# Performance work log

Measured on AMD Instinct MI355X. Metric: run time of the kernel, lower is better.

## Reference

```python
import jax, jax.numpy as jnp
import numpy as np

# KroneckerLinear: W ~= sum_i (A_i kron B_i); efficient path computes, per token,
# Y = sum_i A_i @ X @ B_i^T with X = x.reshape(in1, in2), output flattened as (out1*out2).

IN1, IN2 = 64, 64      # in_factors (in1*in2 = in_features = 4096)
OUT1, OUT2 = 64, 64    # out_factors (out1*out2 = out_features = 4096)
NUM_SUM = 2
BATCH, SEQ = 4, 4096


def setup_inputs() -> dict:
    key = jax.random.key(0)
    kx, ka, kb, kbias = jax.random.split(key, 4)
    x = jax.random.normal(kx, (BATCH, SEQ, IN1 * IN2), dtype=jnp.float32)
    # kaiming-uniform-like scale for small factors
    bound_a = 1.0 / np.sqrt(IN1)
    bound_b = 1.0 / np.sqrt(IN2)
    A = jax.random.uniform(ka, (NUM_SUM, OUT1, IN1), dtype=jnp.float32, minval=-bound_a, maxval=bound_a)
    B = jax.random.uniform(kb, (NUM_SUM, OUT2, IN2), dtype=jnp.float32, minval=-bound_b, maxval=bound_b)
    bound = 1.0 / np.sqrt(IN1 * IN2)
    bias = jax.random.uniform(kbias, (OUT1 * OUT2,), dtype=jnp.float32, minval=-bound, maxval=bound)
    return {"x": x, "A": A, "B": B, "bias": bias}


def reference(x, A, B, bias):
    Bsz, T, _ = x.shape
    X = x.reshape(Bsz, T, IN1, IN2)  # (b, t, i, j)
    # y[b,t,o,p] = sum_s sum_ij A[s,o,i] * X[b,t,i,j] * B[s,p,j]  -> (out1, out2)
    y = jnp.einsum("btij,soi,spj->btop", X, A, B)
    return y.reshape(Bsz, T, OUT1 * OUT2) + bias
```

## Files before the change

kernel.cpp:

```cpp
#include <hip/hip_runtime.h>
#include <hip/hip_bf16.h>

typedef float  f32x4  __attribute__((ext_vector_type(4)));
typedef short  bf16x8 __attribute__((ext_vector_type(8)));

#define NT      16384
#define NBLOCK  256
#define TPS     (NT / NBLOCK)

__device__ __forceinline__ short f2bf(float x) {
  return (short)__builtin_bit_cast(unsigned short, __float2bfloat16(x));
}
__device__ __forceinline__ unsigned packbf2(float a, float b) {
  return (unsigned)(unsigned short)f2bf(a) | ((unsigned)(unsigned short)f2bf(b) << 16);
}

__device__ __forceinline__ void gload16(const float* gp, float* lp) {
  __builtin_amdgcn_global_load_lds((const __attribute__((address_space(1))) void*)gp,
                                   (__attribute__((address_space(3))) void*)lp,
                                   16, 0, 0);
}
__device__ __forceinline__ unsigned ldsaddr(const void* p) {
  return (unsigned)(uintptr_t)(const __attribute__((address_space(3))) void*)p;
}

__device__ __forceinline__ void stageQW(float* XB, const float* gbase, int j, int lane) {
#pragma unroll
  for (int qq = 0; qq < 4; ++qq) {
    const int q = j * 4 + qq;
    const int i = q * 4 + (lane >> 4);
    const float* gp = gbase + i * 64 + (((lane & 15) ^ (i & 7)) << 2);
    gload16(gp, XB + q * 256);
  }
}

__global__ __launch_bounds__(512, 1)
void kron_kernel(const float* __restrict__ x,
                 const float* __restrict__ A,
                 const float* __restrict__ Bm,
                 const float* __restrict__ bias,
                 float* __restrict__ out) {
  __shared__ float  xb[4][4096];
  __shared__ bf16x8 AT[1024];
  __shared__ bf16x8 BT[1024];
  __shared__ unsigned long long Ul[2][2048];

  const int tid  = threadIdx.x;
  const int lane = tid & 63;
  const int w    = tid >> 6;
  const int j    = w & 3;
  const int g    = lane >> 4;
  const int l15  = lane & 15;
  const int blk  = blockIdx.x;
  const bool consumer = (w < 4);

  f32x4 bv[4];
  if (consumer) {
#pragma unroll
    for (int t = 0; t < 4; ++t) {
      const int idx = j * 4 + t;
      const int s = idx >> 3, ot = (idx & 7) >> 1, c = idx & 1;
      const int o = ot * 16 + l15;
      bf16x8 v;
#pragma unroll
      for (int e = 0; e < 8; ++e) {
        const int i = c * 32 + 4 * g + (e & 3) + 16 * (e >> 2);
        v[e] = f2bf(A[s * 4096 + o * 64 + i]);
      }
      AT[idx * 64 + lane] = v;
    }
#pragma unroll
    for (int t = 0; t < 4; ++t) {
      const int idx = j * 4 + t;
      const int s = idx >> 3, pt = (idx & 7) >> 1, jc = idx & 1;
      const int p = pt * 16 + l15;
      bf16x8 v;
#pragma unroll
      for (int e = 0; e < 8; ++e)
        v[e] = f2bf(Bm[s * 4096 + p * 64 + (jc * 32 + 8 * g + e)]);
      BT[idx * 64 + lane] = v;
    }
#pragma unroll
    for (int ot = 0; ot < 4; ++ot)
      bv[ot] = *(const f32x4*)(bias + (ot * 16 + l15) * 64 + j * 16 + 4 * g);
  }
  __syncthreads();

  if (!consumer) {
    stageQW(&xb[0][0], x + ((size_t)blk << 12),            j, lane);
    stageQW(&xb[1][0], x + ((size_t)(blk + NBLOCK) << 12), j, lane);
    asm volatile("s_waitcnt vmcnt(4)" ::: "memory");
  }
  __builtin_amdgcn_s_barrier();

  const unsigned wsw = (unsigned)(2 * ((l15 >> 2) & 1));
  const unsigned q2  = (unsigned)((l15 >> 2) & 1);

  for (int k = 0; k <= TPS; ++k) {
    if (consumer) {
      f32x4 r0[2], r1[2];
      if (k < TPS) {
        const unsigned ba   = ldsaddr(&xb[k & 3][0]);
        const unsigned base = ba + (unsigned)(j * 16 + l15) * 256u;
        const unsigned m    = (unsigned)(l15 & 7);
#pragma unroll
        for (int jc = 0; jc < 2; ++jc) {
          const unsigned c0 = (unsigned)(8 * jc + 2 * g);
          asm volatile("ds_read_b128 %0, %1" : "=v"(r0[jc]) : "v"(base + ((c0 ^ m) << 4)) : "memory");
          asm volatile("ds_read_b128 %0, %1" : "=v"(r1[jc]) : "v"(base + (((c0 + 1u) ^ m) << 4)) : "memory");
        }
      }

      if (k > 0) {
        const unsigned long long* Up = &Ul[(k - 1) & 1][0];
        f32x4 acc[4];
#pragma unroll
        for (int ot = 0; ot < 4; ++ot) acc[ot] = bv[ot];
#pragma unroll
        for (int s = 0; s < 2; ++s) {
          bf16x8 uf[2];
#pragma unroll
          for (int c = 0; c < 2; ++c)
            uf[c] = *reinterpret_cast<const bf16x8*>(
                &Up[((((s * 4 + j) * 4 + g) * 16 + l15) << 2) + 2u * ((unsigned)c ^ q2)]);
#pragma unroll
          for (int ot = 0; ot < 4; ++ot)
#pragma unroll
            for (int c = 0; c < 2; ++c)
              acc[ot] = __builtin_amdgcn_mfma_f32_16x16x32_bf16(
                  uf[c], AT[(s * 8 + ot * 2 + c) * 64 + lane], acc[ot], 0, 0, 0);
        }
        float* ob = out + ((size_t)(blk + (k - 1) * NBLOCK) << 12);
#pragma unroll
        for (int ot = 0; ot < 4; ++ot)
          *(f32x4*)(ob + (ot * 16 + l15) * 64 + j * 16 + 4 * g) = acc[ot];
      }

      if (k < TPS) {
        asm volatile("s_waitcnt lgkmcnt(0)" ::: "memory");
        __builtin_amdgcn_sched_barrier(0);
        bf16x8 xf[2];
#pragma unroll
        for (int jc = 0; jc < 2; ++jc) {
          bf16x8 t;
          t[0]=f2bf(r0[jc][0]); t[1]=f2bf(r0[jc][1]); t[2]=f2bf(r0[jc][2]); t[3]=f2bf(r0[jc][3]);
          t[4]=f2bf(r1[jc][0]); t[5]=f2bf(r1[jc][1]); t[6]=f2bf(r1[jc][2]); t[7]=f2bf(r1[jc][3]);
          xf[jc] = t;
        }
        unsigned long long* Uw = &Ul[k & 1][0];
#pragma unroll
        for (int s = 0; s < 2; ++s) {
#pragma unroll
          for (int pt = 0; pt < 4; ++pt) {
            f32x4 a1 = (f32x4){0.f, 0.f, 0.f, 0.f};
#pragma unroll
            for (int jc = 0; jc < 2; ++jc)
              a1 = __builtin_amdgcn_mfma_f32_16x16x32_bf16(
                  xf[jc], BT[(s * 8 + pt * 2 + jc) * 64 + lane], a1, 0, 0, 0);
            const unsigned lo = packbf2(a1[0], a1[1]);
            const unsigned hi = packbf2(a1[2], a1[3]);
            Uw[((((s * 4 + pt) * 4 + g) * 16 + l15) << 2) + ((unsigned)j ^ wsw)] =
                ((unsigned long long)hi << 32) | lo;
          }
        }
        asm volatile("s_waitcnt lgkmcnt(0)" ::: "memory");
        __builtin_amdgcn_sched_barrier(0);
      }
    } else {
      if (k + 2 < TPS) {
        stageQW(&xb[(k + 2) & 3][0],
                x + ((size_t)(blk + (k + 2) * NBLOCK) << 12), j, lane);
        asm volatile("s_waitcnt vmcnt(4)" ::: "memory");
      } else {
        asm volatile("s_waitcnt vmcnt(0)" ::: "memory");
      }
    }

    if (k < TPS) __builtin_amdgcn_s_barrier();
  }
}

extern "C" void kernel_launch(void* const* d_in, const int* in_sizes, int n_in,
                              void* d_out, int out_size, void* d_ws, size_t ws_size,
                              hipStream_t stream) {
  const float* x    = (const float*)d_in[0];
  const float* A    = (const float*)d_in[1];
  const float* B    = (const float*)d_in[2];
  const float* bias = (const float*)d_in[3];
  float* out        = (float*)d_out;
  kron_kernel<<<dim3(NBLOCK), dim3(512), 0, stream>>>(x, A, B, bias, out);
}
```

Baseline: 112.6 us.

## Process two tokens per iteration with six-deep LDS ring buffer

Restructures the main loop so each iteration handles two tokens: the consumer waves run stage one (X·B^T) for both tokens, then after a barrier run stage two (A·U) for both and store. The producer waves now prefetch two tokens at a time, four tokens ahead, into a six-slot LDS ring instead of a four-slot one. This halves the number of barrier pairs per token and deepens prefetch to hide global load latency. In exchange it uses more LDS (about 96KB for x) and two barriers per iteration, and stage two no longer overlaps with the next token's stage one.

New measurement: 107.6 us. -4.4%, faster.

```diff
diff --git a/kernel.cpp b/kernel.cpp
--- a/kernel.cpp
+++ b/kernel.cpp
@@ -7,6 +7,7 @@
 #define NT      16384
 #define NBLOCK  256
 #define TPS     (NT / NBLOCK)
+#define RING    6
 
 __device__ __forceinline__ short f2bf(float x) {
   return (short)__builtin_bit_cast(unsigned short, __float2bfloat16(x));
@@ -40,7 +41,7 @@
                  const float* __restrict__ Bm,
                  const float* __restrict__ bias,
                  float* __restrict__ out) {
-  __shared__ float  xb[4][4096];
+  __shared__ float  xb[RING][4096];
   __shared__ bf16x8 AT[1024];
   __shared__ bf16x8 BT[1024];
   __shared__ unsigned long long Ul[2][2048];
@@ -87,58 +88,36 @@
   __syncthreads();
 
   if (!consumer) {
-    stageQW(&xb[0][0], x + ((size_t)blk << 12),            j, lane);
-    stageQW(&xb[1][0], x + ((size_t)(blk + NBLOCK) << 12), j, lane);
-    asm volatile("s_waitcnt vmcnt(4)" ::: "memory");
+#pragma unroll
+    for (int p = 0; p < 4; ++p)
+      stageQW(&xb[p][0], x + ((size_t)(blk + p * NBLOCK) << 12), j, lane);
+    asm volatile("s_waitcnt vmcnt(8)" ::: "memory");
   }
   __builtin_amdgcn_s_barrier();
 
   const unsigned wsw = (unsigned)(2 * ((l15 >> 2) & 1));
   const unsigned q2  = (unsigned)((l15 >> 2) & 1);
 
-  for (int k = 0; k <= TPS; ++k) {
+  for (int i = 0; i < TPS / 2; ++i) {
+    const int t0 = 2 * i;
+
     if (consumer) {
-      f32x4 r0[2], r1[2];
-      if (k < TPS) {
-        const unsigned ba   = ldsaddr(&xb[k & 3][0]);
+#pragma unroll
+      for (int h = 0; h < 2; ++h) {
+        const int tok = t0 + h;
+        const unsigned ba   = ldsaddr(&xb[tok % RING][0]);
         const unsigned base = ba + (unsigned)(j * 16 + l15) * 256u;
         const unsigned m    = (unsigned)(l15 & 7);
+        f32x4 r0[2], r1[2];
 #pragma unroll
         for (int jc = 0; jc < 2; ++jc) {
           const unsigned c0 = (unsigned)(8 * jc + 2 * g);
           asm volatile("ds_read_b128 %0, %1" : "=v"(r0[jc]) : "v"(base + ((c0 ^ m) << 4)) : "memory");
           asm volatile("ds_read_b128 %0, %1" : "=v"(r1[jc]) : "v"(base + (((c0 + 1u) ^ m) << 4)) : "memory");
         }
-      }
-
-      if (k > 0) {
-        const unsigned long long* Up = &Ul[(k - 1) & 1][0];
-        f32x4 acc[4];
-#pragma unroll
-        for (int ot = 0; ot < 4; ++ot) acc[ot] = bv[ot];
-#pragma unroll
-        for (int s = 0; s < 2; ++s) {
-          bf16x8 uf[2];
-#pragma unroll
-          for (int c = 0; c < 2; ++c)
-            uf[c] = *reinterpret_cast<const bf16x8*>(
-                &Up[((((s * 4 + j) * 4 + g) * 16 + l15) << 2) + 2u * ((unsigned)c ^ q2)]);
-#pragma unroll
-          for (int ot = 0; ot < 4; ++ot)
-#pragma unroll
-            for (int c = 0; c < 2; ++c)
-              acc[ot] = __builtin_amdgcn_mfma_f32_16x16x32_bf16(
-                  uf[c], AT[(s * 8 + ot * 2 + c) * 64 + lane], acc[ot], 0, 0, 0);
-        }
-        float* ob = out + ((size_t)(blk + (k - 1) * NBLOCK) << 12);
-#pragma unroll
-        for (int ot = 0; ot < 4; ++ot)
-          *(f32x4*)(ob + (ot * 16 + l15) * 64 + j * 16 + 4 * g) = acc[ot];
-      }
-
-      if (k < TPS) {
         asm volatile("s_waitcnt lgkmcnt(0)" ::: "memory");
         __builtin_amdgcn_sched_barrier(0);
+
         bf16x8 xf[2];
 #pragma unroll
         for (int jc = 0; jc < 2; ++jc) {
@@ -147,7 +126,7 @@
           t[4]=f2bf(r1[jc][0]); t[5]=f2bf(r1[jc][1]); t[6]=f2bf(r1[jc][2]); t[7]=f2bf(r1[jc][3]);
           xf[jc] = t;
         }
-        unsigned long long* Uw = &Ul[k & 1][0];
+        unsigned long long* Uw = &Ul[h][0];
 #pragma unroll
         for (int s = 0; s < 2; ++s) {
 #pragma unroll
@@ -163,20 +142,52 @@
                 ((unsigned long long)hi << 32) | lo;
           }
         }
-        asm volatile("s_waitcnt lgkmcnt(0)" ::: "memory");
-        __builtin_amdgcn_sched_barrier(0);
-      }
+      }
+      asm volatile("s_waitcnt lgkmcnt(0)" ::: "memory");
+      __builtin_amdgcn_sched_barrier(0);
     } else {
-      if (k + 2 < TPS) {
-        stageQW(&xb[(k + 2) & 3][0],
-                x + ((size_t)(blk + (k + 2) * NBLOCK) << 12), j, lane);
-        asm volatile("s_waitcnt vmcnt(4)" ::: "memory");
-      } else {
-        asm volatile("s_waitcnt vmcnt(0)" ::: "memory");
-      }
-    }
-
-    if (k < TPS) __builtin_amdgcn_s_barrier();
+      if (t0 + 4 < TPS) {
+        stageQW(&xb[(t0 + 4) % RING][0],
+                x + ((size_t)(blk + (t0 + 4) * NBLOCK) << 12), j, lane);
+        stageQW(&xb[(t0 + 5) % RING][0],
+                x + ((size_t)(blk + (t0 + 5) * NBLOCK) << 12), j, lane);
+      }
+    }
+
+    __builtin_amdgcn_s_barrier();
+
+    if (consumer) {
+#pragma unroll
+      for (int h = 0; h < 2; ++h) {
+        const unsigned long long* Up = &Ul[h][0];
+        f32x4 acc[4];
+#pragma unroll
+        for (int ot = 0; ot < 4; ++ot) acc[ot] = bv[ot];
+#pragma unroll
+        for (int s = 0; s < 2; ++s) {
+          bf16x8 uf[2];
+#pragma unroll
+          for (int c = 0; c < 2; ++c)
+            uf[c] = *reinterpret_cast<const bf16x8*>(
+                &Up[((((s * 4 + j) * 4 + g) * 16 + l15) << 2) + 2u * ((unsigned)c ^ q2)]);
+#pragma unroll
+          for (int ot = 0; ot < 4; ++ot)
+#pragma unroll
+            for (int c = 0; c < 2; ++c)
+              acc[ot] = __builtin_amdgcn_mfma_f32_16x16x32_bf16(
+                  uf[c], AT[(s * 8 + ot * 2 + c) * 64 + lane], acc[ot], 0, 0, 0);
+        }
+        float* ob = out + ((size_t)(blk + (t0 + h) * NBLOCK) << 12);
+#pragma unroll
+        for (int ot = 0; ot < 4; ++ot)
+          *(f32x4*)(ob + (ot * 16 + l15) * 64 + j * 16 + 4 * g) = acc[ot];
+      }
+    } else {
+      if (t0 + 4 < TPS) asm volatile("s_waitcnt vmcnt(8)" ::: "memory");
+      else              asm volatile("s_waitcnt vmcnt(0)" ::: "memory");
+    }
+
+    __builtin_amdgcn_s_barrier();
   }
 }
 
```
